# Performance work log

Hardware: AMD Instinct MI355X
Metric: run time of the kernel (lower is better)

Reference implementation:

```python
import jax, jax.numpy as jnp
import numpy as np

N = 100000
E = 1600000
D = 128
EIG = 32
NUM_MOTIFS = 64
EPS = 1e-8  # torch cosine_similarity eps


def setup_inputs() -> dict:
    key = jax.random.key(0)
    ks = jax.random.split(key, 12)
    return {
        "q": jax.random.normal(ks[0], (N, D), jnp.float32),
        "k": jax.random.normal(ks[1], (N, D), jnp.float32),
        "v": jax.random.normal(ks[2], (N, D), jnp.float32),
        "eigs": jax.random.normal(ks[3], (N, EIG), jnp.float32),
        "motif_adj_vals": jax.random.uniform(ks[4], (E,), jnp.float32),
        "lambda0": jax.random.normal(ks[5], (1,), jnp.float32) * 0.1,
        "gamma": jax.random.normal(ks[6], (1,), jnp.float32) * 0.1,
        "motif_emb_w": jax.random.uniform(ks[7], (NUM_MOTIFS, 1), jnp.float32),
        "row": jax.random.randint(ks[8], (E,), 0, N, jnp.int32),
        "col": jax.random.randint(ks[9], (E,), 0, N, jnp.int32),
        "motif_ids": jax.random.randint(ks[10], (N,), 0, NUM_MOTIFS, jnp.int32),
    }


def _sparse_softmax(vals, row, n):
    # softmax of per-edge values grouped by destination/row index
    m = jax.ops.segment_max(vals, row, num_segments=n)
    e = jnp.exp(vals - m[row])
    z = jax.ops.segment_sum(e, row, num_segments=n)
    return e / z[row]


def reference(q, k, v, eigs, motif_adj_vals, lambda0, gamma, motif_emb_w,
              row, col, motif_ids):
    sqrt_dim = 1.0 / jnp.sqrt(jnp.asarray(q.shape[1], q.dtype))
    # edge-wise q.k dot product, scaled
    x = jnp.sum(q[row] * k[col], axis=-1) * sqrt_dim          # [E]
    # eig branch (args.model contains 'eig'); note original does NOT scale by sqrt_eig
    y = jnp.sum(eigs[row] * eigs[col], axis=-1)               # [E]
    s0 = x + jnp.exp(lambda0[0]) * y
    # motif branch: embedding lookup + cosine similarity along the edge dim (dim=0)
    me = motif_emb_w[motif_ids][:, 0]                          # [N]
    a, b = me[row], me[col]                                    # [E]
    sim = jnp.sum(a * b) / (jnp.maximum(jnp.linalg.norm(a), EPS)
                            * jnp.maximum(jnp.linalg.norm(b), EPS))
    s1 = motif_adj_vals * gamma[0] * sim                       # [E]
    n = q.shape[0]
    attn = 0.5 * (_sparse_softmax(s0, row, n) + _sparse_softmax(s1, row, n))
    # sparse-dense matmul: out[r] = sum_e attn_e * v[col_e]
    return jax.ops.segment_sum(attn[:, None] * v[col], row, num_segments=n)
```

## Files before the change

kernel.cpp:

```cpp
#include <hip/hip_runtime.h>
#include <math.h>

#define N_NODES 100000
#define N_EDGES 1600000
#define DIM 128
#define EIGD 32
#define CS_EPS 1e-8f

#define B1 256
#define CHUNK 6250
#define NB 391

static const size_t OFF_REC    = 0;
static const size_t OFF_SE     = 12800000;
static const size_t OFF_GH     = 25600000;
static const size_t OFF_BSTART = 26000384;
static const size_t OFF_GPART  = 26001952;
static const size_t OFF_OFFS   = 26006048;
static const size_t OFF_SCAL   = 26406064;
static const size_t OFF_KB     = 26406080;
static const size_t OFF_VB     = 52006080;
static const size_t OFF_EB     = 77606080;

__device__ __forceinline__ unsigned short f2bf(float f) {
    unsigned u = __float_as_uint(f);
    unsigned r = (u + 0x7fffu + ((u >> 16) & 1u)) >> 16;
    return (unsigned short)r;
}
__device__ __forceinline__ float blo(unsigned w) { return __uint_as_float(w << 16); }
__device__ __forceinline__ float bhi(unsigned w) { return __uint_as_float(w & 0xffff0000u); }

#define K4C 3200000
#define E4C 800000

__global__ void __launch_bounds__(256) ka_cvt(
        const float* __restrict__ k, const float* __restrict__ v,
        const float* __restrict__ eigs,
        ushort* __restrict__ kb, ushort* __restrict__ vb,
        ushort* __restrict__ eb) {
    int i = blockIdx.x * blockDim.x + threadIdx.x;
    const float* src; ushort* dst; int j;
    if (i < K4C)            { src = k;    dst = kb; j = i; }
    else if (i < 2 * K4C)   { src = v;    dst = vb; j = i - K4C; }
    else if (i < 2*K4C+E4C) { src = eigs; dst = eb; j = i - 2 * K4C; }
    else return;
    float4 f = ((const float4*)src)[j];
    ushort4 o;
    o.x = f2bf(f.x); o.y = f2bf(f.y); o.z = f2bf(f.z); o.w = f2bf(f.w);
    ((ushort4*)dst)[j] = o;
}

__global__ void __launch_bounds__(256) kb_hist(
        const int* __restrict__ row, const int* __restrict__ col,
        const float* __restrict__ motif_w, const int* __restrict__ motif_ids,
        int* __restrict__ gh, float4* __restrict__ gpart) {
    __shared__ int hist[NB];
    __shared__ float wlds[64];
    __shared__ float red[3][4];
    const int t = threadIdx.x, b = blockIdx.x;
    for (int i = t; i < NB; i += 256) hist[i] = 0;
    if (t < 64) wlds[t] = motif_w[t];
    __syncthreads();

    const int e0 = b * CHUNK, e1 = min(N_EDGES, e0 + CHUNK);
    float sab = 0.f, saa = 0.f, sbb = 0.f;
    for (int e = e0 + t; e < e1; e += 256) {
        int r = row[e], c = col[e];
        atomicAdd(&hist[r >> 8], 1);
        float mr = wlds[motif_ids[r]], mc = wlds[motif_ids[c]];
        sab += mr * mc; saa += mr * mr; sbb += mc * mc;
    }
#pragma unroll
    for (int off = 32; off >= 1; off >>= 1) {
        sab += __shfl_xor(sab, off);
        saa += __shfl_xor(saa, off);
        sbb += __shfl_xor(sbb, off);
    }
    int lane = t & 63, wid = t >> 6;
    if (lane == 0) { red[0][wid] = sab; red[1][wid] = saa; red[2][wid] = sbb; }
    __syncthreads();
    if (t == 0) {
        float a = 0.f, bb = 0.f, cc = 0.f;
#pragma unroll
        for (int i = 0; i < 4; i++) { a += red[0][i]; bb += red[1][i]; cc += red[2][i]; }
        gpart[b] = make_float4(a, bb, cc, 0.f);
    }
    __syncthreads();
    for (int i = t; i < NB; i += 256) gh[b * NB + i] = hist[i];
}

__global__ void __launch_bounds__(512) ke_scan(
        int* __restrict__ gh, int* __restrict__ bstart,
        const float4* __restrict__ gpart, const float* __restrict__ gamma,
        float* __restrict__ scal, int* __restrict__ offs) {
    const int t = threadIdx.x;
    __shared__ int tot[512];
    int mytot = 0;
    if (t < NB) {
        int run = 0;
        for (int b = 0; b < B1; b++) {
            int v = gh[b * NB + t];
            gh[b * NB + t] = run;
            run += v;
        }
        mytot = run;
    }
    tot[t] = mytot;
    __syncthreads();
    for (int off = 1; off < 512; off <<= 1) {
        int v = (t >= off) ? tot[t - off] : 0;
        __syncthreads();
        tot[t] += v;
        __syncthreads();
    }
    if (t < NB) bstart[t] = tot[t] - mytot;
    if (t == NB - 1) {
        bstart[NB] = tot[t];
        offs[N_NODES] = tot[t];
    }

    float sab = 0.f, saa = 0.f, sbb = 0.f;
    for (int i = t; i < B1; i += 512) {
        float4 g = gpart[i];
        sab += g.x; saa += g.y; sbb += g.z;
    }
#pragma unroll
    for (int off = 32; off >= 1; off >>= 1) {
        sab += __shfl_xor(sab, off);
        saa += __shfl_xor(saa, off);
        sbb += __shfl_xor(sbb, off);
    }
    __shared__ float red[3][8];
    int lane = t & 63, wid = t >> 6;
    if (lane == 0) { red[0][wid] = sab; red[1][wid] = saa; red[2][wid] = sbb; }
    __syncthreads();
    if (t == 0) {
        float a = 0.f, bb = 0.f, cc = 0.f;
#pragma unroll
        for (int i = 0; i < 8; i++) { a += red[0][i]; bb += red[1][i]; cc += red[2][i]; }
        float na = sqrtf(bb); if (na < CS_EPS) na = CS_EPS;
        float nb2 = sqrtf(cc); if (nb2 < CS_EPS) nb2 = CS_EPS;
        scal[0] = gamma[0] * (a / (na * nb2));
    }
}

__global__ void __launch_bounds__(256) kd_coarse(
        const int* __restrict__ row, const int* __restrict__ col,
        const float* __restrict__ adj, const int* __restrict__ gh,
        const int* __restrict__ bstart, int2* __restrict__ rec) {
    __shared__ int cur[NB];
    const int t = threadIdx.x, b = blockIdx.x;
    for (int i = t; i < NB; i += 256) cur[i] = bstart[i] + gh[b * NB + i];
    __syncthreads();
    const int e0 = b * CHUNK, e1 = min(N_EDGES, e0 + CHUNK);
    for (int e = e0 + t; e < e1; e += 256) {
        int r = row[e];
        int pos = atomicAdd(&cur[r >> 8], 1);
        rec[pos] = make_int2(col[e] | ((r & 255) << 17), __float_as_int(adj[e]));
    }
}

__global__ void __launch_bounds__(256) kf_fine(
        const int2* __restrict__ rec, const int* __restrict__ bstart,
        int* __restrict__ offs, float2* __restrict__ se) {
    __shared__ int hist[256], sc[256], cur[256];
    const int t = threadIdx.x, b = blockIdx.x;
    hist[t] = 0;
    __syncthreads();
    const int s = bstart[b], e1 = bstart[b + 1];
    for (int i = s + t; i < e1; i += 256) {
        int rl = (rec[i].x >> 17) & 255;
        atomicAdd(&hist[rl], 1);
    }
    __syncthreads();
    int v = hist[t];
    sc[t] = v;
    __syncthreads();
    for (int off = 1; off < 256; off <<= 1) {
        int w = (t >= off) ? sc[t - off] : 0;
        __syncthreads();
        sc[t] += w;
        __syncthreads();
    }
    int excl = sc[t] - v;
    int rowg = b * 256 + t;
    if (rowg < N_NODES) offs[rowg] = s + excl;
    cur[t] = s + excl;
    __syncthreads();
    for (int i = s + t; i < e1; i += 256) {
        int2 rc = rec[i];
        int rl = (rc.x >> 17) & 255;
        int pos = atomicAdd(&cur[rl], 1);
        se[pos] = make_float2(__int_as_float(rc.x & 0x1FFFF), __int_as_float(rc.y));
    }
}

__global__ void __launch_bounds__(256) k4_flash(
        const float* __restrict__ q, const ushort* __restrict__ kb,
        const ushort* __restrict__ eb, const ushort* __restrict__ vb,
        const float* __restrict__ lambda0, const int* __restrict__ offs,
        const float2* __restrict__ se, const float* __restrict__ scal,
        float* __restrict__ out) {
    const int tid  = threadIdx.x;
    const int lane = tid & 63;
    const int wid  = tid >> 6;
    const int r = blockIdx.x * 4 + wid;
    if (r >= N_NODES) return;
    const int l16 = lane & 15;
    const int grp = lane >> 4;
    const float inv_sqrt_d = 0.08838834764831843f;

    const int start = offs[r], end = offs[r + 1];
    if (end == start) {
        ((float2*)(out + (size_t)r * DIM))[lane] = make_float2(0.f, 0.f);
        return;
    }

    const float el0 = expf(lambda0[0]);
    const float cs  = scal[0];

    const float4* qp = (const float4*)(q + (size_t)r * DIM);
    const float4 qa = qp[l16 * 2];
    const float4 qc = qp[l16 * 2 + 1];
    const unsigned erw = *(const unsigned*)(eb + (size_t)r * EIGD + l16 * 2);
    const float er0 = blo(erw), er1 = bhi(erw);

    float m0 = -INFINITY, z0 = 0.f, m1 = -INFINITY, z1 = 0.f;
    float2 acc0 = make_float2(0.f, 0.f), acc1 = make_float2(0.f, 0.f);

    for (int base = start; base < end; base += 4) {
        int e = base + grp;
        float s0p = -INFINITY, s1v = -INFINITY;
        int c = 0;
        if (e < end) {
            float2 ea = se[e];
            c = __float_as_int(ea.x);
            s1v = cs * ea.y;
            const uint4 kw = *(const uint4*)(kb + (size_t)c * DIM + l16 * 8);
            float x;
            x = qa.x * blo(kw.x);
            x = fmaf(qa.y, bhi(kw.x), x);
            x = fmaf(qa.z, blo(kw.y), x);
            x = fmaf(qa.w, bhi(kw.y), x);
            x = fmaf(qc.x, blo(kw.z), x);
            x = fmaf(qc.y, bhi(kw.z), x);
            x = fmaf(qc.z, blo(kw.w), x);
            x = fmaf(qc.w, bhi(kw.w), x);
            const unsigned ecw = *(const unsigned*)(eb + (size_t)c * EIGD + l16 * 2);
            float y = er0 * blo(ecw) + er1 * bhi(ecw);
            s0p = x * inv_sqrt_d + el0 * y;
        }
#pragma unroll
        for (int off = 8; off >= 1; off >>= 1) s0p += __shfl_xor(s0p, off);

        float s00 = __shfl(s0p, 0),  s01 = __shfl(s0p, 16);
        float s02 = __shfl(s0p, 32), s03 = __shfl(s0p, 48);
        float s10 = __shfl(s1v, 0),  s11 = __shfl(s1v, 16);
        float s12 = __shfl(s1v, 32), s13 = __shfl(s1v, 48);
        int   c0  = __shfl(c, 0),    c1  = __shfl(c, 16);
        int   c2  = __shfl(c, 32),   c3  = __shfl(c, 48);
        int cnt = end - base;

        float nm0 = fmaxf(m0, fmaxf(fmaxf(s00, s01), fmaxf(s02, s03)));
        float r0  = __expf(m0 - nm0);
        float w00 = __expf(s00 - nm0);
        float w01 = __expf(s01 - nm0);
        float w02 = __expf(s02 - nm0);
        float w03 = __expf(s03 - nm0);
        z0 = z0 * r0 + w00 + w01 + w02 + w03;
        m0 = nm0;

        float nm1 = fmaxf(m1, fmaxf(fmaxf(s10, s11), fmaxf(s12, s13)));
        float r1  = __expf(m1 - nm1);
        float w10 = __expf(s10 - nm1);
        float w11 = __expf(s11 - nm1);
        float w12 = __expf(s12 - nm1);
        float w13 = __expf(s13 - nm1);
        z1 = z1 * r1 + w10 + w11 + w12 + w13;
        m1 = nm1;

        acc0.x *= r0; acc0.y *= r0;
        acc1.x *= r1; acc1.y *= r1;
        {
            unsigned vw = *(const unsigned*)(vb + (size_t)c0 * DIM + lane * 2);
            float vx = blo(vw), vy = bhi(vw);
            acc0.x = fmaf(w00, vx, acc0.x); acc0.y = fmaf(w00, vy, acc0.y);
            acc1.x = fmaf(w10, vx, acc1.x); acc1.y = fmaf(w10, vy, acc1.y);
        }
        if (cnt > 1) {
            unsigned vw = *(const unsigned*)(vb + (size_t)c1 * DIM + lane * 2);
            float vx = blo(vw), vy = bhi(vw);
            acc0.x = fmaf(w01, vx, acc0.x); acc0.y = fmaf(w01, vy, acc0.y);
            acc1.x = fmaf(w11, vx, acc1.x); acc1.y = fmaf(w11, vy, acc1.y);
        }
        if (cnt > 2) {
            unsigned vw = *(const unsigned*)(vb + (size_t)c2 * DIM + lane * 2);
            float vx = blo(vw), vy = bhi(vw);
            acc0.x = fmaf(w02, vx, acc0.x); acc0.y = fmaf(w02, vy, acc0.y);
            acc1.x = fmaf(w12, vx, acc1.x); acc1.y = fmaf(w12, vy, acc1.y);
        }
        if (cnt > 3) {
            unsigned vw = *(const unsigned*)(vb + (size_t)c3 * DIM + lane * 2);
            float vx = blo(vw), vy = bhi(vw);
            acc0.x = fmaf(w03, vx, acc0.x); acc0.y = fmaf(w03, vy, acc0.y);
            acc1.x = fmaf(w13, vx, acc1.x); acc1.y = fmaf(w13, vy, acc1.y);
        }
    }

    float iz0 = 1.f / z0, iz1 = 1.f / z1;
    float2 o = make_float2(0.5f * (acc0.x * iz0 + acc1.x * iz1),
                           0.5f * (acc0.y * iz0 + acc1.y * iz1));
    ((float2*)(out + (size_t)r * DIM))[lane] = o;
}

extern "C" void kernel_launch(void* const* d_in, const int* in_sizes, int n_in,
                              void* d_out, int out_size, void* d_ws, size_t ws_size,
                              hipStream_t stream) {
    const float* q        = (const float*)d_in[0];
    const float* k        = (const float*)d_in[1];
    const float* v        = (const float*)d_in[2];
    const float* eigs     = (const float*)d_in[3];
    const float* adj      = (const float*)d_in[4];
    const float* lambda0  = (const float*)d_in[5];
    const float* gamma    = (const float*)d_in[6];
    const float* motif_w  = (const float*)d_in[7];
    const int*   row      = (const int*)d_in[8];
    const int*   col      = (const int*)d_in[9];
    const int*   motif_ids= (const int*)d_in[10];
    float* out = (float*)d_out;

    char* ws = (char*)d_ws;
    int2*   rec    = (int2*)(ws + OFF_REC);
    float2* se     = (float2*)(ws + OFF_SE);
    int*    gh     = (int*)(ws + OFF_GH);
    int*    bstart = (int*)(ws + OFF_BSTART);
    float4* gpart  = (float4*)(ws + OFF_GPART);
    int*    offs   = (int*)(ws + OFF_OFFS);
    float*  scal   = (float*)(ws + OFF_SCAL);
    ushort* kb     = (ushort*)(ws + OFF_KB);
    ushort* vb     = (ushort*)(ws + OFF_VB);
    ushort* eb     = (ushort*)(ws + OFF_EB);

    hipLaunchKernelGGL(ka_cvt, dim3((2 * K4C + E4C + 255) / 256), dim3(256), 0, stream,
                       k, v, eigs, kb, vb, eb);
    hipLaunchKernelGGL(kb_hist, dim3(B1), dim3(256), 0, stream,
                       row, col, motif_w, motif_ids, gh, gpart);
    hipLaunchKernelGGL(ke_scan, dim3(1), dim3(512), 0, stream,
                       gh, bstart, gpart, gamma, scal, offs);
    hipLaunchKernelGGL(kd_coarse, dim3(B1), dim3(256), 0, stream,
                       row, col, adj, gh, bstart, rec);
    hipLaunchKernelGGL(kf_fine, dim3(NB), dim3(256), 0, stream,
                       rec, bstart, offs, se);
    hipLaunchKernelGGL(k4_flash, dim3((N_NODES + 3) / 4), dim3(256), 0, stream,
                       q, kb, eb, vb, lambda0, offs, se, scal, out);
}
```

Measured before the change: 478.1 us.

## Parallelize bucket scan, raise histogram blocks, prefetch gathers in flash aggregation

The histogram pass now uses 1024 blocks instead of 256, and the single-block serial column scan is split into a parallel per-bucket scan kernel followed by a small global scan. The flash aggregation kernel is restructured so that each 16-lane group owns one edge and accumulates 8 output dims in registers. Its K, V and eig gathers for the next edge are software-pipelined one iteration ahead, and the four group partial softmax states are merged with shuffles at the end. The aim is to remove the serial scan bottleneck and hide gather latency in the main kernel, at the cost of more registers, an extra launch, and per-edge branching in the online softmax.

```diff
diff --git a/kernel.cpp b/kernel.cpp
--- a/kernel.cpp
+++ b/kernel.cpp
@@ -7,20 +7,21 @@
 #define EIGD 32
 #define CS_EPS 1e-8f
 
-#define B1 256
-#define CHUNK 6250
+#define B1 1024
+#define CHUNK 1563
 #define NB 391
 
 static const size_t OFF_REC    = 0;
 static const size_t OFF_SE     = 12800000;
-static const size_t OFF_GH     = 25600000;
-static const size_t OFF_BSTART = 26000384;
-static const size_t OFF_GPART  = 26001952;
-static const size_t OFF_OFFS   = 26006048;
-static const size_t OFF_SCAL   = 26406064;
-static const size_t OFF_KB     = 26406080;
-static const size_t OFF_VB     = 52006080;
-static const size_t OFF_EB     = 77606080;
+static const size_t OFF_GH     = 12800000;
+static const size_t OFF_BSTART = 25600000;
+static const size_t OFF_BTOT   = 25601600;
+static const size_t OFF_GPART  = 25603200;
+static const size_t OFF_OFFS   = 25619584;
+static const size_t OFF_SCAL   = 26019600;
+static const size_t OFF_KB     = 26019616;
+static const size_t OFF_VB     = 51619616;
+static const size_t OFF_EB     = 77219616;
 
 __device__ __forceinline__ unsigned short f2bf(float f) {
     unsigned u = __float_as_uint(f);
@@ -89,23 +90,40 @@
     for (int i = t; i < NB; i += 256) gh[b * NB + i] = hist[i];
 }
 
-__global__ void __launch_bounds__(512) ke_scan(
-        int* __restrict__ gh, int* __restrict__ bstart,
+__global__ void __launch_bounds__(256) ks_scanA(
+        int* __restrict__ gh, int* __restrict__ btot) {
+    const int colb = blockIdx.x;
+    const int t = threadIdx.x;
+    int v0 = gh[(t * 4 + 0) * NB + colb];
+    int v1 = gh[(t * 4 + 1) * NB + colb];
+    int v2 = gh[(t * 4 + 2) * NB + colb];
+    int v3 = gh[(t * 4 + 3) * NB + colb];
+    int tot4 = v0 + v1 + v2 + v3;
+    __shared__ int sc[256];
+    sc[t] = tot4;
+    __syncthreads();
+    for (int off = 1; off < 256; off <<= 1) {
+        int w = (t >= off) ? sc[t - off] : 0;
+        __syncthreads();
+        sc[t] += w;
+        __syncthreads();
+    }
+    int excl = sc[t] - tot4;
+    gh[(t * 4 + 0) * NB + colb] = excl;
+    gh[(t * 4 + 1) * NB + colb] = excl + v0;
+    gh[(t * 4 + 2) * NB + colb] = excl + v0 + v1;
+    gh[(t * 4 + 3) * NB + colb] = excl + v0 + v1 + v2;
+    if (t == 255) btot[colb] = excl + tot4;
+}
+
+__global__ void __launch_bounds__(512) ks_scanB(
+        const int* __restrict__ btot, int* __restrict__ bstart,
         const float4* __restrict__ gpart, const float* __restrict__ gamma,
         float* __restrict__ scal, int* __restrict__ offs) {
     const int t = threadIdx.x;
     __shared__ int tot[512];
-    int mytot = 0;
-    if (t < NB) {
-        int run = 0;
-        for (int b = 0; b < B1; b++) {
-            int v = gh[b * NB + t];
-            gh[b * NB + t] = run;
-            run += v;
-        }
-        mytot = run;
-    }
-    tot[t] = mytot;
+    int my = (t < NB) ? btot[t] : 0;
+    tot[t] = my;
     __syncthreads();
     for (int off = 1; off < 512; off <<= 1) {
         int v = (t >= off) ? tot[t - off] : 0;
@@ -113,17 +131,15 @@
         tot[t] += v;
         __syncthreads();
     }
-    if (t < NB) bstart[t] = tot[t] - mytot;
+    if (t < NB) bstart[t] = tot[t] - my;
     if (t == NB - 1) {
         bstart[NB] = tot[t];
         offs[N_NODES] = tot[t];
     }
 
-    float sab = 0.f, saa = 0.f, sbb = 0.f;
-    for (int i = t; i < B1; i += 512) {
-        float4 g = gpart[i];
-        sab += g.x; saa += g.y; sbb += g.z;
-    }
+    float4 g0 = gpart[t];
+    float4 g1 = gpart[t + 512];
+    float sab = g0.x + g1.x, saa = g0.y + g1.y, sbb = g0.z + g1.z;
 #pragma unroll
     for (int off = 32; off >= 1; off >>= 1) {
         sab += __shfl_xor(sab, off);
@@ -211,12 +227,13 @@
     const float inv_sqrt_d = 0.08838834764831843f;
 
     const int start = offs[r], end = offs[r + 1];
+    float2* outp = (float2*)(out + (size_t)r * DIM);
     if (end == start) {
-        ((float2*)(out + (size_t)r * DIM))[lane] = make_float2(0.f, 0.f);
+        outp[l16 * 4 + grp] = make_float2(0.f, 0.f);
         return;
     }
 
-    const float el0 = expf(lambda0[0]);
+    const float el0 = __expf(lambda0[0]);
     const float cs  = scal[0];
 
     const float4* qp = (const float4*)(q + (size_t)r * DIM);
@@ -225,92 +242,123 @@
     const unsigned erw = *(const unsigned*)(eb + (size_t)r * EIGD + l16 * 2);
     const float er0 = blo(erw), er1 = bhi(erw);
 
-    float m0 = -INFINITY, z0 = 0.f, m1 = -INFINITY, z1 = 0.f;
-    float2 acc0 = make_float2(0.f, 0.f), acc1 = make_float2(0.f, 0.f);
+    const float NEG = -1e30f;
+    float m0 = NEG, z0 = 0.f, m1 = NEG, z1 = 0.f;
+    float a0[8], a1[8];
+#pragma unroll
+    for (int j = 0; j < 8; j++) { a0[j] = 0.f; a1[j] = 0.f; }
+
+    const int last = end - 1;
+    float2 ea_c = se[min(start + grp, last)];
+    int c_c = __float_as_int(ea_c.x);
+    uint4 kw_c = *(const uint4*)(kb + (size_t)c_c * DIM + l16 * 8);
+    uint4 vw_c = *(const uint4*)(vb + (size_t)c_c * DIM + l16 * 8);
+    unsigned ecw_c = *(const unsigned*)(eb + (size_t)c_c * EIGD + l16 * 2);
+    float2 ea_n = ea_c;
+    if (start + 4 < end) ea_n = se[min(start + 4 + grp, last)];
 
     for (int base = start; base < end; base += 4) {
-        int e = base + grp;
-        float s0p = -INFINITY, s1v = -INFINITY;
-        int c = 0;
-        if (e < end) {
-            float2 ea = se[e];
-            c = __float_as_int(ea.x);
-            s1v = cs * ea.y;
-            const uint4 kw = *(const uint4*)(kb + (size_t)c * DIM + l16 * 8);
-            float x;
-            x = qa.x * blo(kw.x);
-            x = fmaf(qa.y, bhi(kw.x), x);
-            x = fmaf(qa.z, blo(kw.y), x);
-            x = fmaf(qa.w, bhi(kw.y), x);
-            x = fmaf(qc.x, blo(kw.z), x);
-            x = fmaf(qc.y, bhi(kw.z), x);
-            x = fmaf(qc.z, blo(kw.w), x);
-            x = fmaf(qc.w, bhi(kw.w), x);
-            const unsigned ecw = *(const unsigned*)(eb + (size_t)c * EIGD + l16 * 2);
-            float y = er0 * blo(ecw) + er1 * bhi(ecw);
-            s0p = x * inv_sqrt_d + el0 * y;
+        const bool has1 = (base + 4) < end;
+        const bool has2 = (base + 8) < end;
+        uint4 kw_n = kw_c, vw_n = vw_c; unsigned ecw_n = ecw_c;
+        if (has1) {
+            int c_n = __float_as_int(ea_n.x);
+            kw_n = *(const uint4*)(kb + (size_t)c_n * DIM + l16 * 8);
+            vw_n = *(const uint4*)(vb + (size_t)c_n * DIM + l16 * 8);
+            ecw_n = *(const unsigned*)(eb + (size_t)c_n * EIGD + l16 * 2);
         }
+        float2 ea_n2 = ea_n;
+        if (has2) ea_n2 = se[min(base + 8 + grp, last)];
+
+        const bool act = (base + grp) < end;
+        float x;
+        x = qa.x * blo(kw_c.x);
+        x = fmaf(qa.y, bhi(kw_c.x), x);
+        x = fmaf(qa.z, blo(kw_c.y), x);
+        x = fmaf(qa.w, bhi(kw_c.y), x);
+        x = fmaf(qc.x, blo(kw_c.z), x);
+        x = fmaf(qc.y, bhi(kw_c.z), x);
+        x = fmaf(qc.z, blo(kw_c.w), x);
+        x = fmaf(qc.w, bhi(kw_c.w), x);
+        float y = er0 * blo(ecw_c) + er1 * bhi(ecw_c);
+        float s0p = fmaf(el0, y, x * inv_sqrt_d);
 #pragma unroll
         for (int off = 8; off >= 1; off >>= 1) s0p += __shfl_xor(s0p, off);
-
-        float s00 = __shfl(s0p, 0),  s01 = __shfl(s0p, 16);
-        float s02 = __shfl(s0p, 32), s03 = __shfl(s0p, 48);
-        float s10 = __shfl(s1v, 0),  s11 = __shfl(s1v, 16);
-        float s12 = __shfl(s1v, 32), s13 = __shfl(s1v, 48);
-        int   c0  = __shfl(c, 0),    c1  = __shfl(c, 16);
-        int   c2  = __shfl(c, 32),   c3  = __shfl(c, 48);
-        int cnt = end - base;
-
-        float nm0 = fmaxf(m0, fmaxf(fmaxf(s00, s01), fmaxf(s02, s03)));
-        float r0  = __expf(m0 - nm0);
-        float w00 = __expf(s00 - nm0);
-        float w01 = __expf(s01 - nm0);
-        float w02 = __expf(s02 - nm0);
-        float w03 = __expf(s03 - nm0);
-        z0 = z0 * r0 + w00 + w01 + w02 + w03;
-        m0 = nm0;
-
-        float nm1 = fmaxf(m1, fmaxf(fmaxf(s10, s11), fmaxf(s12, s13)));
-        float r1  = __expf(m1 - nm1);
-        float w10 = __expf(s10 - nm1);
-        float w11 = __expf(s11 - nm1);
-        float w12 = __expf(s12 - nm1);
-        float w13 = __expf(s13 - nm1);
-        z1 = z1 * r1 + w10 + w11 + w12 + w13;
-        m1 = nm1;
-
-        acc0.x *= r0; acc0.y *= r0;
-        acc1.x *= r1; acc1.y *= r1;
-        {
-            unsigned vw = *(const unsigned*)(vb + (size_t)c0 * DIM + lane * 2);
-            float vx = blo(vw), vy = bhi(vw);
-            acc0.x = fmaf(w00, vx, acc0.x); acc0.y = fmaf(w00, vy, acc0.y);
-            acc1.x = fmaf(w10, vx, acc1.x); acc1.y = fmaf(w10, vy, acc1.y);
+        float s1v = cs * ea_c.y;
+
+        unsigned vws0 = vw_c.x, vws1 = vw_c.y, vws2 = vw_c.z, vws3 = vw_c.w;
+        if (act) {
+            if (s0p > m0) {
+                float r0 = __expf(m0 - s0p);
+                z0 *= r0;
+#pragma unroll
+                for (int j = 0; j < 8; j++) a0[j] *= r0;
+                m0 = s0p;
+            }
+            float w0 = __expf(s0p - m0);
+            z0 += w0;
+            if (s1v > m1) {
+                float r1 = __expf(m1 - s1v);
+                z1 *= r1;
+#pragma unroll
+                for (int j = 0; j < 8; j++) a1[j] *= r1;
+                m1 = s1v;
+            }
+            float w1 = __expf(s1v - m1);
+            z1 += w1;
+            {
+                float lo, hi;
+                lo = blo(vws0); hi = bhi(vws0);
+                a0[0] = fmaf(w0, lo, a0[0]); a0[1] = fmaf(w0, hi, a0[1]);
+                a1[0] = fmaf(w1, lo, a1[0]); a1[1] = fmaf(w1, hi, a1[1]);
+                lo = blo(vws1); hi = bhi(vws1);
+                a0[2] = fmaf(w0, lo, a0[2]); a0[3] = fmaf(w0, hi, a0[3]);
+                a1[2] = fmaf(w1, lo, a1[2]); a1[3] = fmaf(w1, hi, a1[3]);
+                lo = blo(vws2); hi = bhi(vws2);
+                a0[4] = fmaf(w0, lo, a0[4]); a0[5] = fmaf(w0, hi, a0[5]);
+                a1[4] = fmaf(w1, lo, a1[4]); a1[5] = fmaf(w1, hi, a1[5]);
+                lo = blo(vws3); hi = bhi(vws3);
+                a0[6] = fmaf(w0, lo, a0[6]); a0[7] = fmaf(w0, hi, a0[7]);
+                a1[6] = fmaf(w1, lo, a1[6]); a1[7] = fmaf(w1, hi, a1[7]);
+            }
         }
-        if (cnt > 1) {
-            unsigned vw = *(const unsigned*)(vb + (size_t)c1 * DIM + lane * 2);
-            float vx = blo(vw), vy = bhi(vw);
-            acc0.x = fmaf(w01, vx, acc0.x); acc0.y = fmaf(w01, vy, acc0.y);
-            acc1.x = fmaf(w11, vx, acc1.x); acc1.y = fmaf(w11, vy, acc1.y);
+        ea_c = ea_n; ea_n = ea_n2;
+        kw_c = kw_n; vw_c = vw_n; ecw_c = ecw_n;
+    }
+
+#pragma unroll
+    for (int off = 16; off <= 32; off <<= 1) {
+        float mo = __shfl_xor(m0, off);
+        float zo = __shfl_xor(z0, off);
+        float M  = fmaxf(m0, mo);
+        float sa = __expf(m0 - M), sb = __expf(mo - M);
+        z0 = z0 * sa + zo * sb;
+#pragma unroll
+        for (int j = 0; j < 8; j++) {
+            float ao = __shfl_xor(a0[j], off);
+            a0[j] = a0[j] * sa + ao * sb;
         }
-        if (cnt > 2) {
-            unsigned vw = *(const unsigned*)(vb + (size_t)c2 * DIM + lane * 2);
-            float vx = blo(vw), vy = bhi(vw);
-            acc0.x = fmaf(w02, vx, acc0.x); acc0.y = fmaf(w02, vy, acc0.y);
-            acc1.x = fmaf(w12, vx, acc1.x); acc1.y = fmaf(w12, vy, acc1.y);
+        m0 = M;
+        float mo1 = __shfl_xor(m1, off);
+        float zo1 = __shfl_xor(z1, off);
+        float M1  = fmaxf(m1, mo1);
+        float sa1 = __expf(m1 - M1), sb1 = __expf(mo1 - M1);
+        z1 = z1 * sa1 + zo1 * sb1;
+#pragma unroll
+        for (int j = 0; j < 8; j++) {
+            float ao = __shfl_xor(a1[j], off);
+            a1[j] = a1[j] * sa1 + ao * sb1;
         }
-        if (cnt > 3) {
-            unsigned vw = *(const unsigned*)(vb + (size_t)c3 * DIM + lane * 2);
-            float vx = blo(vw), vy = bhi(vw);
-            acc0.x = fmaf(w03, vx, acc0.x); acc0.y = fmaf(w03, vy, acc0.y);
-            acc1.x = fmaf(w13, vx, acc1.x); acc1.y = fmaf(w13, vy, acc1.y);
-        }
+        m1 = M1;
     }
 
     float iz0 = 1.f / z0, iz1 = 1.f / z1;
-    float2 o = make_float2(0.5f * (acc0.x * iz0 + acc1.x * iz1),
-                           0.5f * (acc0.y * iz0 + acc1.y * iz1));
-    ((float2*)(out + (size_t)r * DIM))[lane] = o;
+    float b00 = grp == 0 ? a0[0] : grp == 1 ? a0[2] : grp == 2 ? a0[4] : a0[6];
+    float b01 = grp == 0 ? a0[1] : grp == 1 ? a0[3] : grp == 2 ? a0[5] : a0[7];
+    float b10 = grp == 0 ? a1[0] : grp == 1 ? a1[2] : grp == 2 ? a1[4] : a1[6];
+    float b11 = grp == 0 ? a1[1] : grp == 1 ? a1[3] : grp == 2 ? a1[5] : a1[7];
+    outp[l16 * 4 + grp] = make_float2(0.5f * (b00 * iz0 + b10 * iz1),
+                                      0.5f * (b01 * iz0 + b11 * iz1));
 }
 
 extern "C" void kernel_launch(void* const* d_in, const int* in_sizes, int n_in,
@@ -334,6 +382,7 @@
     float2* se     = (float2*)(ws + OFF_SE);
     int*    gh     = (int*)(ws + OFF_GH);
     int*    bstart = (int*)(ws + OFF_BSTART);
+    int*    btot   = (int*)(ws + OFF_BTOT);
     float4* gpart  = (float4*)(ws + OFF_GPART);
     int*    offs   = (int*)(ws + OFF_OFFS);
     float*  scal   = (float*)(ws + OFF_SCAL);
@@ -345,8 +394,10 @@
                        k, v, eigs, kb, vb, eb);
     hipLaunchKernelGGL(kb_hist, dim3(B1), dim3(256), 0, stream,
                        row, col, motif_w, motif_ids, gh, gpart);
-    hipLaunchKernelGGL(ke_scan, dim3(1), dim3(512), 0, stream,
-                       gh, bstart, gpart, gamma, scal, offs);
+    hipLaunchKernelGGL(ks_scanA, dim3(NB), dim3(256), 0, stream,
+                       gh, btot);
+    hipLaunchKernelGGL(ks_scanB, dim3(1), dim3(512), 0, stream,
+                       btot, bstart, gpart, gamma, scal, offs);
     hipLaunchKernelGGL(kd_coarse, dim3(B1), dim3(256), 0, stream,
                        row, col, adj, gh, bstart, rec);
     hipLaunchKernelGGL(kf_fine, dim3(NB), dim3(256), 0, stream,
```

After: 477.3 us. Within noise of the previous version (-0.2%).

## Parallelize bucket scan across blocks, raise histogram blocks, stage fine sort in LDS

Applied to the files above, without the earlier changes.

Replaces the single-block serial column scan over the per-block histograms with a multi-block scan (one block per bucket) followed by a small single-block scan of bucket totals. The coarse histogram/scatter now runs with 1024 blocks instead of 256, which gives more parallelism on the edge passes. The fine per-bucket sort stages records in shared memory and writes the output contiguously, avoiding a second global read and scattered global writes. This adds a kernel launch and a large LDS footprint per block, with a global fallback when a bucket exceeds the capacity. The gh region now overlaps the se region, which is only safe because se is written after gh is last read.

```diff
diff --git a/kernel.cpp b/kernel.cpp
--- a/kernel.cpp
+++ b/kernel.cpp
@@ -7,20 +7,22 @@
 #define EIGD 32
 #define CS_EPS 1e-8f
 
-#define B1 256
-#define CHUNK 6250
+#define B1 1024
+#define CHUNK 1563
 #define NB 391
+#define FCAP 4800
 
 static const size_t OFF_REC    = 0;
 static const size_t OFF_SE     = 12800000;
-static const size_t OFF_GH     = 25600000;
-static const size_t OFF_BSTART = 26000384;
-static const size_t OFF_GPART  = 26001952;
-static const size_t OFF_OFFS   = 26006048;
-static const size_t OFF_SCAL   = 26406064;
-static const size_t OFF_KB     = 26406080;
-static const size_t OFF_VB     = 52006080;
-static const size_t OFF_EB     = 77606080;
+static const size_t OFF_GH     = 12800000;
+static const size_t OFF_BSTART = 25600000;
+static const size_t OFF_BTOT   = 25601600;
+static const size_t OFF_GPART  = 25603200;
+static const size_t OFF_OFFS   = 25619584;
+static const size_t OFF_SCAL   = 26019600;
+static const size_t OFF_KB     = 26019616;
+static const size_t OFF_VB     = 51619616;
+static const size_t OFF_EB     = 77219616;
 
 __device__ __forceinline__ unsigned short f2bf(float f) {
     unsigned u = __float_as_uint(f);
@@ -89,23 +91,40 @@
     for (int i = t; i < NB; i += 256) gh[b * NB + i] = hist[i];
 }
 
-__global__ void __launch_bounds__(512) ke_scan(
-        int* __restrict__ gh, int* __restrict__ bstart,
+__global__ void __launch_bounds__(256) ks_scanA(
+        int* __restrict__ gh, int* __restrict__ btot) {
+    const int colb = blockIdx.x;
+    const int t = threadIdx.x;
+    int v0 = gh[(t * 4 + 0) * NB + colb];
+    int v1 = gh[(t * 4 + 1) * NB + colb];
+    int v2 = gh[(t * 4 + 2) * NB + colb];
+    int v3 = gh[(t * 4 + 3) * NB + colb];
+    int tot4 = v0 + v1 + v2 + v3;
+    __shared__ int sc[256];
+    sc[t] = tot4;
+    __syncthreads();
+    for (int off = 1; off < 256; off <<= 1) {
+        int w = (t >= off) ? sc[t - off] : 0;
+        __syncthreads();
+        sc[t] += w;
+        __syncthreads();
+    }
+    int excl = sc[t] - tot4;
+    gh[(t * 4 + 0) * NB + colb] = excl;
+    gh[(t * 4 + 1) * NB + colb] = excl + v0;
+    gh[(t * 4 + 2) * NB + colb] = excl + v0 + v1;
+    gh[(t * 4 + 3) * NB + colb] = excl + v0 + v1 + v2;
+    if (t == 255) btot[colb] = excl + tot4;
+}
+
+__global__ void __launch_bounds__(512) ks_scanB(
+        const int* __restrict__ btot, int* __restrict__ bstart,
         const float4* __restrict__ gpart, const float* __restrict__ gamma,
         float* __restrict__ scal, int* __restrict__ offs) {
     const int t = threadIdx.x;
     __shared__ int tot[512];
-    int mytot = 0;
-    if (t < NB) {
-        int run = 0;
-        for (int b = 0; b < B1; b++) {
-            int v = gh[b * NB + t];
-            gh[b * NB + t] = run;
-            run += v;
-        }
-        mytot = run;
-    }
-    tot[t] = mytot;
+    int my = (t < NB) ? btot[t] : 0;
+    tot[t] = my;
     __syncthreads();
     for (int off = 1; off < 512; off <<= 1) {
         int v = (t >= off) ? tot[t - off] : 0;
@@ -113,17 +132,15 @@
         tot[t] += v;
         __syncthreads();
     }
-    if (t < NB) bstart[t] = tot[t] - mytot;
+    if (t < NB) bstart[t] = tot[t] - my;
     if (t == NB - 1) {
         bstart[NB] = tot[t];
         offs[N_NODES] = tot[t];
     }
 
-    float sab = 0.f, saa = 0.f, sbb = 0.f;
-    for (int i = t; i < B1; i += 512) {
-        float4 g = gpart[i];
-        sab += g.x; saa += g.y; sbb += g.z;
-    }
+    float4 g0 = gpart[t];
+    float4 g1 = gpart[t + 512];
+    float sab = g0.x + g1.x, saa = g0.y + g1.y, sbb = g0.z + g1.z;
 #pragma unroll
     for (int off = 32; off >= 1; off >>= 1) {
         sab += __shfl_xor(sab, off);
@@ -160,38 +177,65 @@
     }
 }
 
-__global__ void __launch_bounds__(256) kf_fine(
+__global__ void __launch_bounds__(512) kf_fine(
         const int2* __restrict__ rec, const int* __restrict__ bstart,
         int* __restrict__ offs, float2* __restrict__ se) {
     __shared__ int hist[256], sc[256], cur[256];
+    __shared__ int2 buf[FCAP];
+    __shared__ int2 buf2[FCAP];
     const int t = threadIdx.x, b = blockIdx.x;
-    hist[t] = 0;
+    if (t < 256) hist[t] = 0;
     __syncthreads();
     const int s = bstart[b], e1 = bstart[b + 1];
-    for (int i = s + t; i < e1; i += 256) {
-        int rl = (rec[i].x >> 17) & 255;
-        atomicAdd(&hist[rl], 1);
-    }
-    __syncthreads();
-    int v = hist[t];
-    sc[t] = v;
+    const int cnt = e1 - s;
+    const bool ldsok = (cnt <= FCAP);
+    if (ldsok) {
+        for (int i = t; i < cnt; i += 512) {
+            int2 rc = rec[s + i];
+            buf[i] = rc;
+            atomicAdd(&hist[(rc.x >> 17) & 255], 1);
+        }
+    } else {
+        for (int i = t; i < cnt; i += 512)
+            atomicAdd(&hist[(rec[s + i].x >> 17) & 255], 1);
+    }
+    __syncthreads();
+    int v = 0;
+    if (t < 256) { v = hist[t]; sc[t] = v; }
     __syncthreads();
     for (int off = 1; off < 256; off <<= 1) {
-        int w = (t >= off) ? sc[t - off] : 0;
-        __syncthreads();
-        sc[t] += w;
-        __syncthreads();
-    }
-    int excl = sc[t] - v;
-    int rowg = b * 256 + t;
-    if (rowg < N_NODES) offs[rowg] = s + excl;
-    cur[t] = s + excl;
-    __syncthreads();
-    for (int i = s + t; i < e1; i += 256) {
-        int2 rc = rec[i];
-        int rl = (rc.x >> 17) & 255;
-        int pos = atomicAdd(&cur[rl], 1);
-        se[pos] = make_float2(__int_as_float(rc.x & 0x1FFFF), __int_as_float(rc.y));
+        int w = 0;
+        if (t < 256 && t >= off) w = sc[t - off];
+        __syncthreads();
+        if (t < 256) sc[t] += w;
+        __syncthreads();
+    }
+    if (t < 256) {
+        int excl = sc[t] - v;
+        int rowg = b * 256 + t;
+        if (rowg < N_NODES) offs[rowg] = s + excl;
+        cur[t] = ldsok ? excl : (s + excl);
+    }
+    __syncthreads();
+    if (ldsok) {
+        for (int i = t; i < cnt; i += 512) {
+            int2 rc = buf[i];
+            int rl = (rc.x >> 17) & 255;
+            int pos = atomicAdd(&cur[rl], 1);
+            buf2[pos] = make_int2(rc.x & 0x1FFFF, rc.y);
+        }
+        __syncthreads();
+        for (int i = t; i < cnt; i += 512) {
+            int2 o = buf2[i];
+            se[s + i] = make_float2(__int_as_float(o.x), __int_as_float(o.y));
+        }
+    } else {
+        for (int i = t; i < cnt; i += 512) {
+            int2 rc = rec[s + i];
+            int rl = (rc.x >> 17) & 255;
+            int pos = atomicAdd(&cur[rl], 1);
+            se[pos] = make_float2(__int_as_float(rc.x & 0x1FFFF), __int_as_float(rc.y));
+        }
     }
 }
 
@@ -334,6 +378,7 @@
     float2* se     = (float2*)(ws + OFF_SE);
     int*    gh     = (int*)(ws + OFF_GH);
     int*    bstart = (int*)(ws + OFF_BSTART);
+    int*    btot   = (int*)(ws + OFF_BTOT);
     float4* gpart  = (float4*)(ws + OFF_GPART);
     int*    offs   = (int*)(ws + OFF_OFFS);
     float*  scal   = (float*)(ws + OFF_SCAL);
@@ -345,11 +390,13 @@
                        k, v, eigs, kb, vb, eb);
     hipLaunchKernelGGL(kb_hist, dim3(B1), dim3(256), 0, stream,
                        row, col, motif_w, motif_ids, gh, gpart);
-    hipLaunchKernelGGL(ke_scan, dim3(1), dim3(512), 0, stream,
-                       gh, bstart, gpart, gamma, scal, offs);
+    hipLaunchKernelGGL(ks_scanA, dim3(NB), dim3(256), 0, stream,
+                       gh, btot);
+    hipLaunchKernelGGL(ks_scanB, dim3(1), dim3(512), 0, stream,
+                       btot, bstart, gpart, gamma, scal, offs);
     hipLaunchKernelGGL(kd_coarse, dim3(B1), dim3(256), 0, stream,
                        row, col, adj, gh, bstart, rec);
-    hipLaunchKernelGGL(kf_fine, dim3(NB), dim3(256), 0, stream,
+    hipLaunchKernelGGL(kf_fine, dim3(NB), dim3(512), 0, stream,
                        rec, bstart, offs, se);
     hipLaunchKernelGGL(k4_flash, dim3((N_NODES + 3) / 4), dim3(256), 0, stream,
                        q, kb, eb, vb, lambda0, offs, se, scal, out);
```

After: 478.7 us. Within noise of the previous version (+0.1%).
